# Optimization experiments

Hardware: AMD Instinct MI355X
Metric: run time of the kernel (lower is better)

Reference implementation:

```python
import math
import jax, jax.numpy as jnp
import numpy as np

B, T, C = 4, 2048, 1024
N_HEAD = 16
HEAD_DIM = C // N_HEAD

def setup_inputs() -> dict:
    key = jax.random.key(0)
    k0, k1, k2, k3, k4 = jax.random.split(key, 5)
    s = 1.0 / math.sqrt(C)
    return {
        "x": jax.random.normal(k0, (B, T, C), dtype=jnp.float32),
        "W_q": jax.random.normal(k1, (C, C), dtype=jnp.float32) * s,
        "W_k": jax.random.normal(k2, (C, C), dtype=jnp.float32) * s,
        "W_v": jax.random.normal(k3, (C, C), dtype=jnp.float32) * s,
        "W_o": jax.random.normal(k4, (C, C), dtype=jnp.float32) * s,
    }

def reference(x, W_q, W_k, W_v, W_o):
    b, t, c = x.shape
    h, hd = N_HEAD, HEAD_DIM
    # nn.Linear(y) = y @ W.T ; project and split heads -> [B, H, T, hd]
    q = (x @ W_q.T).reshape(b, t, h, hd).transpose(0, 2, 1, 3)
    k = (x @ W_k.T).reshape(b, t, h, hd).transpose(0, 2, 1, 3)
    v = (x @ W_v.T).reshape(b, t, h, hd).transpose(0, 2, 1, 3)
    # scores [B, H, T, T], causal mask, stable softmax
    attn = jnp.einsum('bhqd,bhkd->bhqk', q, k) / math.sqrt(hd)
    causal = jnp.tril(jnp.ones((t, t), dtype=bool))
    attn = jnp.where(causal[None, None], attn, -jnp.inf)
    attn = jax.nn.softmax(attn, axis=-1)
    out = jnp.einsum('bhqk,bhkd->bhqd', attn, v)
    out = out.transpose(0, 2, 1, 3).reshape(b, t, c)
    return out @ W_o.T
```

## Files before the change

kernel.cpp:

```cpp
#include <hip/hip_runtime.h>
#include <math.h>

#define Bsz 4
#define Tsz 2048
#define Csz 1024
#define NH  16
#define HD  64

typedef short bf16x8 __attribute__((ext_vector_type(8)));
typedef float f32x4  __attribute__((ext_vector_type(4)));
typedef unsigned short u16;
typedef unsigned int uint;

__device__ __forceinline__ u16 f2bf(float f) {
    union { float f; unsigned u; } v; v.f = f;
    unsigned r = v.u + 0x7fffu + ((v.u >> 16) & 1u);
    return (u16)(r >> 16);
}

__device__ __forceinline__ uint pkbf(float a, float b) {
    union { float f; uint u; } x, y; x.f = a; y.f = b;
    return ((x.u + 0x8000u) >> 16) | ((y.u + 0x8000u) & 0xFFFF0000u);
}

__device__ __forceinline__ void glds16(const u16* g, u16* l) {
    __builtin_amdgcn_global_load_lds(
        (const __attribute__((address_space(1))) void*)g,
        (__attribute__((address_space(3))) void*)l, 16, 0, 0);
}

__global__ void cast_kernel(const float* __restrict__ src, u16* __restrict__ dst, int n) {
    int i = (blockIdx.x * blockDim.x + threadIdx.x) * 8;
    if (i + 8 <= n) {
        float4 a = *(const float4*)(src + i);
        float4 b = *(const float4*)(src + i + 4);
        bf16x8 o;
        o[0] = (short)f2bf(a.x); o[1] = (short)f2bf(a.y);
        o[2] = (short)f2bf(a.z); o[3] = (short)f2bf(a.w);
        o[4] = (short)f2bf(b.x); o[5] = (short)f2bf(b.y);
        o[6] = (short)f2bf(b.z); o[7] = (short)f2bf(b.w);
        *(bf16x8*)(dst + i) = o;
    } else {
        for (; i < n; i++) dst[i] = f2bf(src[i]);
    }
}

__global__ void cast4_kernel(const float* __restrict__ s0, const float* __restrict__ s1,
                             const float* __restrict__ s2, const float* __restrict__ s3,
                             u16* __restrict__ dst) {
    const int NW = Csz * Csz;
    int i = (blockIdx.x * blockDim.x + threadIdx.x) * 8;
    int m = i >> 20;
    int local = i & (NW - 1);
    const float* src = (m == 0) ? s0 : (m == 1) ? s1 : (m == 2) ? s2 : s3;
    float4 a = *(const float4*)(src + local);
    float4 b = *(const float4*)(src + local + 4);
    bf16x8 o;
    o[0] = (short)f2bf(a.x); o[1] = (short)f2bf(a.y);
    o[2] = (short)f2bf(a.z); o[3] = (short)f2bf(a.w);
    o[4] = (short)f2bf(b.x); o[5] = (short)f2bf(b.y);
    o[6] = (short)f2bf(b.z); o[7] = (short)f2bf(b.w);
    *(bf16x8*)(dst + i) = o;
}


#define G8_SLOTSZ 32768
#define G8_MATSZ  16384
#define G8_KHSZ    8192

#define G8_STAGE(SLOT, MAT, KH, KT, PTR)                                             \
    { _Pragma("unroll")                                                              \
      for (int rho = 0; rho < 2; rho++) {                                            \
        const int row = rho * 128 + (tid >> 2);                                      \
        const int sc = (tid & 3) ^ ((row >> 1) & 3);                                 \
        glds16((PTR) + (size_t)row * 1024 + (KT) * 64 + (KH) * 32 + sc * 8,          \
               lds + (SLOT) * G8_SLOTSZ + (MAT) * G8_MATSZ + (KH) * G8_KHSZ +        \
                     rho * 4096 + wave * 512);                                       \
    } }

#define G8_PHASE(SLOT, KH, MH, STAGE)                                                \
    {                                                                                \
        __builtin_amdgcn_s_barrier();                                                \
        asm volatile("" ::: "memory");                                               \
        STAGE                                                                        \
        const u16* abase = lds + (SLOT) * G8_SLOTSZ + (KH) * G8_KHSZ;                \
        const u16* bbase = abase + G8_MATSZ;                                         \
        if ((MH) == 0) {                                                             \
            _Pragma("unroll")                                                        \
            for (int j = 0; j < 4; j++) {                                            \
                const int nr = wcb + j * 16 + lr;                                    \
                bfrag[j] = *(const bf16x8*)(bbase + nr * 32 +                        \
                                            ((lq ^ ((nr >> 1) & 3)) * 8));           \
            }                                                                        \
        }                                                                            \
        bf16x8 afr[4];                                                               \
        _Pragma("unroll")                                                            \
        for (int i = 0; i < 4; i++) {                                                \
            const int ar = wrb + ((MH) * 4 + i) * 16 + lr;                           \
            afr[i] = *(const bf16x8*)(abase + ar * 32 +                              \
                                      ((lq ^ ((ar >> 1) & 3)) * 8));                 \
        }                                                                            \
        asm volatile("" ::: "memory");                                               \
        __builtin_amdgcn_s_setprio(1);                                               \
        _Pragma("unroll")                                                            \
        for (int i = 0; i < 4; i++)                                                  \
            _Pragma("unroll")                                                        \
            for (int j = 0; j < 4; j++)                                              \
                acc[(MH) * 4 + i][j] = __builtin_amdgcn_mfma_f32_16x16x32_bf16(      \
                    afr[i], bfrag[j], acc[(MH) * 4 + i][j], 0, 0, 0);                \
        __builtin_amdgcn_s_setprio(0);                                               \
    }

#define G8_VM(N) asm volatile("s_waitcnt vmcnt(" #N ")" ::: "memory")

#define G8_BODY(AP_, BP_)                                                            \
    __shared__ u16 lds[65536];                                                       \
    const int tid = threadIdx.x;                                                     \
    const int wave = tid >> 6, lane = tid & 63;                                      \
    const int lr = lane & 15, lq = lane >> 4;                                        \
    const int wrb = (wave >> 2) * 128, wcb = (wave & 3) * 64;                        \
    f32x4 acc[8][4] = {};                                                            \
    bf16x8 bfrag[4];                                                                 \
    G8_STAGE(0, 0, 0, 0, AP_) G8_STAGE(0, 1, 0, 0, BP_)                              \
    G8_STAGE(0, 0, 1, 0, AP_) G8_STAGE(0, 1, 1, 0, BP_)                              \
    G8_STAGE(1, 0, 0, 1, AP_) G8_STAGE(1, 1, 0, 1, BP_)                              \
    for (int t = 0; t < 16; t++) {                                                   \
        const int s = t & 1;                                                         \
        if (t == 15) { G8_VM(4); } else { G8_VM(8); }                                \
        G8_PHASE(s, 0, 0, if (t < 15) G8_STAGE(s ^ 1, 0, 1, t + 1, AP_))             \
        G8_PHASE(s, 0, 1, if (t < 15) G8_STAGE(s ^ 1, 1, 1, t + 1, BP_))             \
        if (t == 15) { G8_VM(0); } else { G8_VM(8); }                                \
        G8_PHASE(s, 1, 0, if (t < 14) G8_STAGE(s, 0, 0, t + 2, AP_))                 \
        G8_PHASE(s, 1, 1, if (t < 14) G8_STAGE(s, 1, 0, t + 2, BP_))                 \
    }

__global__ __launch_bounds__(512, 2)
void gemm_qkv(const u16* __restrict__ A, const u16* __restrict__ Bm,
              u16* __restrict__ Qo, u16* __restrict__ Ko, u16* __restrict__ Vo,
              float qscale) {
    const int wg = blockIdx.x;
    const int chunk = wg & 7, pos = wg >> 3;
    const int m0 = ((chunk >> 1) * 8 + pos / 6) * 256;
    const int n0 = ((chunk & 1) * 6 + pos % 6) * 256;
    const u16* Ap = A  + (size_t)m0 * 1024;
    const u16* Bp = Bm + (size_t)n0 * 1024;

    G8_BODY(Ap, Bp)

    const int sel = n0 >> 10;
    if (sel == 2) {
        #pragma unroll
        for (int mi = 0; mi < 8; mi++) {
            #pragma unroll
            for (int ni = 0; ni < 4; ni++) {
                int m = m0 + wrb + mi * 16 + lq * 4;
                int b = m >> 11, tt = m & (Tsz - 1);
                int n = (n0 & 1023) + wcb + ni * 16 + lr;
                int h = n >> 6, d = n & (HD - 1);
                uint2 pk;
                pk.x = pkbf(acc[mi][ni][0], acc[mi][ni][1]);
                pk.y = pkbf(acc[mi][ni][2], acc[mi][ni][3]);
                *(uint2*)(&Vo[(((size_t)b * NH + h) * HD + d) * Tsz + tt]) = pk;
            }
        }
    } else {
        const float scale = (sel == 0) ? qscale : 1.0f;
        u16* dst = (sel == 0) ? Qo : Ko;
        #pragma unroll
        for (int mi = 0; mi < 8; mi++)
            #pragma unroll
            for (int ni = 0; ni < 4; ni++)
                #pragma unroll
                for (int r = 0; r < 4; r++) {
                    int m = m0 + wrb + mi * 16 + lq * 4 + r;
                    int n = (n0 & 1023) + wcb + ni * 16 + lr;
                    int b = m >> 11, tt = m & (Tsz - 1);
                    int h = n >> 6,  d = n & (HD - 1);
                    dst[(((size_t)b * NH + h) * Tsz + tt) * HD + d] = f2bf(acc[mi][ni][r] * scale);
                }
    }
}

__global__ __launch_bounds__(512, 2)
void gemm_out(const u16* __restrict__ A, const u16* __restrict__ Bm,
              float* __restrict__ out) {
    const int wg = blockIdx.x;
    const int chunk = wg & 7, pos = wg >> 3;
    const int m0 = (chunk * 4 + (pos >> 2)) * 256;
    const int n0 = (pos & 3) * 256;
    const u16* Ap = A  + (size_t)m0 * 1024;
    const u16* Bp = Bm + (size_t)n0 * 1024;

    G8_BODY(Ap, Bp)

    #pragma unroll
    for (int mi = 0; mi < 8; mi++)
        #pragma unroll
        for (int ni = 0; ni < 4; ni++)
            #pragma unroll
            for (int r = 0; r < 4; r++) {
                int m = m0 + wrb + mi * 16 + lq * 4 + r;
                int n = n0 + wcb + ni * 16 + lr;
                out[(size_t)m * Csz + n] = acc[mi][ni][r];
            }
}

#define LDT  72
#define LDTP 68

__global__ __launch_bounds__(256, 4)
void attn_kernel(const u16* __restrict__ Q, const u16* __restrict__ Kb,
                 const u16* __restrict__ Vt, u16* __restrict__ O) {
    __shared__ u16 sK[64 * LDT];
    __shared__ u16 sV[64 * LDT];
    __shared__ u16 sP[4][16 * LDTP];
    const int tid  = threadIdx.x;
    const int wave = tid >> 6, lane = tid & 63;
    const int lr = lane & 15, lq = lane >> 4;
    const int bh = blockIdx.x;
    const int qa = blockIdx.y;
    const int qc = 31 - qa;
    const int ta = qa * 64, tc = qc * 64;

    const u16* Qp = Q  + (size_t)bh * Tsz * HD;
    const u16* Kp = Kb + (size_t)bh * Tsz * HD;
    const u16* Vp = Vt + (size_t)bh * HD * Tsz;

    bf16x8 qfA0 = *(const bf16x8*)(Qp + (size_t)(ta + wave * 16 + lr) * HD + lq * 8);
    bf16x8 qfA1 = *(const bf16x8*)(Qp + (size_t)(ta + wave * 16 + lr) * HD + 32 + lq * 8);
    bf16x8 qfC0 = *(const bf16x8*)(Qp + (size_t)(tc + wave * 16 + lr) * HD + lq * 8);
    bf16x8 qfC1 = *(const bf16x8*)(Qp + (size_t)(tc + wave * 16 + lr) * HD + 32 + lq * 8);

    f32x4 accOA[4] = {}, accOC[4] = {};
    f32x4 accLA = {}, accLC = {};

    bf16x8 ones;
    #pragma unroll
    for (int i = 0; i < 8; i++) ones[i] = (short)0x3F80;

    const int strow = tid >> 3;
    const int stcol = (tid & 7) * 8;
    const u16* gK0 = Kp + (size_t)strow * HD + stcol;
    const u16* gK1 = gK0 + 32 * HD;
    const u16* gV0 = Vp + (size_t)strow * Tsz + stcol;
    const u16* gV1 = gV0 + 32 * Tsz;
    u16* lK0 = sK + strow * LDT + stcol;  u16* lK1 = lK0 + 32 * LDT;
    u16* lV0 = sV + strow * LDT + stcol;  u16* lV1 = lV0 + 32 * LDT;

    bf16x8 pK0 = *(const bf16x8*)(gK0);
    bf16x8 pK1 = *(const bf16x8*)(gK1);
    bf16x8 pV0 = *(const bf16x8*)(gV0);
    bf16x8 pV1 = *(const bf16x8*)(gV1);

#define PROCESS(T0, QF0, QF1, ACCO, ACCL, DIAG)                                       \
    {                                                                                 \
        f32x4 accS[4];                                                                \
        _Pragma("unroll")                                                             \
        for (int j = 0; j < 4; j++) {                                                 \
            bf16x8 b0 = *(const bf16x8*)(sK + (j * 16 + lr) * LDT + lq * 8);          \
            bf16x8 b1 = *(const bf16x8*)(sK + (j * 16 + lr) * LDT + 32 + lq * 8);     \
            f32x4 z = {};                                                             \
            z = __builtin_amdgcn_mfma_f32_16x16x32_bf16(QF0, b0, z, 0, 0, 0);         \
            z = __builtin_amdgcn_mfma_f32_16x16x32_bf16(QF1, b1, z, 0, 0, 0);         \
            accS[j] = z;                                                              \
        }                                                                             \
        _Pragma("unroll")                                                             \
        for (int r = 0; r < 4; r++) {                                                 \
            const int rowg = (T0) + wave * 16 + lq * 4 + r;                           \
            _Pragma("unroll")                                                         \
            for (int j = 0; j < 4; j++) {                                             \
                float v = accS[j][r];                                                 \
                if (DIAG && (kb * 64 + j * 16 + lr > rowg)) v = -200.0f;              \
                union { float f; uint u; } e;                                         \
                e.f = __builtin_amdgcn_exp2f(v);                                      \
                sP[wave][(lq * 4 + r) * LDTP + j * 16 + lr] = (u16)(e.u >> 16);       \
            }                                                                         \
        }                                                                             \
        _Pragma("unroll")                                                             \
        for (int ks = 0; ks < 2; ks++) {                                              \
            bf16x8 pf = *(const bf16x8*)(&sP[wave][0] + lr * LDTP + ks * 32 + lq * 8);\
            ACCL = __builtin_amdgcn_mfma_f32_16x16x32_bf16(pf, ones, ACCL, 0, 0, 0);  \
            _Pragma("unroll")                                                         \
            for (int j = 0; j < 4; j++) {                                             \
                bf16x8 vf = *(const bf16x8*)(sV + (j * 16 + lr) * LDT + ks * 32 + lq * 8); \
                ACCO[j] = __builtin_amdgcn_mfma_f32_16x16x32_bf16(pf, vf, ACCO[j], 0, 0, 0); \
            }                                                                         \
        }                                                                             \
    }

    for (int kb = 0; kb <= qc; kb++) {
        __syncthreads();
        *(bf16x8*)lK0 = pK0; *(bf16x8*)lK1 = pK1;
        *(bf16x8*)lV0 = pV0; *(bf16x8*)lV1 = pV1;
        __syncthreads();
        if (kb < qc) {
            pK0 = *(const bf16x8*)(gK0 + (size_t)(kb + 1) * 64 * HD);
            pK1 = *(const bf16x8*)(gK1 + (size_t)(kb + 1) * 64 * HD);
            pV0 = *(const bf16x8*)(gV0 + (kb + 1) * 64);
            pV1 = *(const bf16x8*)(gV1 + (kb + 1) * 64);
        }
        if (kb <= qa) PROCESS(ta, qfA0, qfA1, accOA, accLA, (kb == qa));
        PROCESS(tc, qfC0, qfC1, accOC, accLC, (kb == qc));
    }
#undef PROCESS

    const int b = bh >> 4, h = bh & 15;
    #pragma unroll
    for (int j = 0; j < 4; j++) {
        #pragma unroll
        for (int r = 0; r < 4; r++) {
            int t = wave * 16 + lq * 4 + r;
            int d = j * 16 + lr;
            O[((size_t)b * Tsz + ta + t) * Csz + h * HD + d] = f2bf(accOA[j][r] / accLA[r]);
            O[((size_t)b * Tsz + tc + t) * Csz + h * HD + d] = f2bf(accOC[j][r] / accLC[r]);
        }
    }
}

extern "C" void kernel_launch(void* const* d_in, const int* in_sizes, int n_in,
                              void* d_out, int out_size, void* d_ws, size_t ws_size,
                              hipStream_t stream) {
    const float* x  = (const float*)d_in[0];
    const float* Wq = (const float*)d_in[1];
    const float* Wk = (const float*)d_in[2];
    const float* Wv = (const float*)d_in[3];
    const float* Wo = (const float*)d_in[4];
    float* out = (float*)d_out;

    const size_t NX = (size_t)Bsz * Tsz * Csz;
    const size_t NW = (size_t)Csz * Csz;

    char* ws = (char*)d_ws;
    u16* xb   = (u16*)ws; ws += NX * 2;
    u16* wqkv = (u16*)ws; ws += 3 * NW * 2;
    u16* wob  = (u16*)ws; ws += NW * 2;
    u16* qbuf = (u16*)ws; ws += NX * 2;
    u16* kbuf = (u16*)ws; ws += NX * 2;
    u16* vtb  = (u16*)ws; ws += NX * 2;
    u16* abuf = (u16*)ws; ws += NX * 2;

    cast_kernel<<<dim3((unsigned)(NX / 2048)), 256, 0, stream>>>(x, xb, (int)NX);
    cast4_kernel<<<dim3((unsigned)(4 * NW / 2048)), 256, 0, stream>>>(Wq, Wk, Wv, Wo, wqkv);

    const float qscale = 0.125f * 1.44269504088896340736f;
    gemm_qkv<<<dim3(384), 512, 0, stream>>>(xb, wqkv, qbuf, kbuf, vtb, qscale);

    attn_kernel<<<dim3(Bsz * NH, 16), 256, 0, stream>>>(qbuf, kbuf, vtb, abuf);

    gemm_out<<<dim3(128), 512, 0, stream>>>(abuf, wob, out);
}
```

Baseline: 251.7 us.

## Shrink GEMM tiles to 128x256, raise priority on attention MFMAs, specialize diagonal branches

Both projection GEMMs change from 256x256 output tiles to 128x256, which halves the accumulators and LDS per workgroup and doubles the grid (768 and 256 blocks). The aim is to fill all CUs better, since the output GEMM previously launched only 128 blocks on a device with far more CUs. In exchange, each tile reuses less data per byte loaded. The attention kernel also wraps its MFMA sections in s_setprio and splits the per-block branch so the causal mask is compiled in only for diagonal blocks.

```diff
diff --git a/kernel.cpp b/kernel.cpp
--- a/kernel.cpp
+++ b/kernel.cpp
@@ -64,41 +64,41 @@
 }
 
 
-#define G8_SLOTSZ 32768
-#define G8_MATSZ  16384
-#define G8_KHSZ    8192
-
-#define G8_STAGE(SLOT, MAT, KH, KT, PTR)                                             \
-    { _Pragma("unroll")                                                              \
-      for (int rho = 0; rho < 2; rho++) {                                            \
-        const int row = rho * 128 + (tid >> 2);                                      \
-        const int sc = (tid & 3) ^ ((row >> 1) & 3);                                 \
-        glds16((PTR) + (size_t)row * 1024 + (KT) * 64 + (KH) * 32 + sc * 8,          \
-               lds + (SLOT) * G8_SLOTSZ + (MAT) * G8_MATSZ + (KH) * G8_KHSZ +        \
-                     rho * 4096 + wave * 512);                                       \
-    } }
-
-#define G8_PHASE(SLOT, KH, MH, STAGE)                                                \
+#define G2_SS 24576
+
+#define G2_STAGEA(SLOT, KH, KT, PTR) {                                               \
+    const int row_ = tid >> 2;                                                       \
+    const int sc_ = (tid & 3) ^ ((row_ >> 1) & 3);                                   \
+    glds16((PTR) + (size_t)row_ * 1024 + (KT) * 64 + (KH) * 32 + sc_ * 8,            \
+           lds + (SLOT) * G2_SS + (KH) * 4096 + wave * 512); }
+
+#define G2_STAGEB(SLOT, KH, KT, PTR) {                                               \
+    _Pragma("unroll")                                                                \
+    for (int rho = 0; rho < 2; rho++) {                                              \
+        const int row_ = rho * 128 + (tid >> 2);                                     \
+        const int sc_ = (tid & 3) ^ ((row_ >> 1) & 3);                               \
+        glds16((PTR) + (size_t)row_ * 1024 + (KT) * 64 + (KH) * 32 + sc_ * 8,        \
+               lds + (SLOT) * G2_SS + 8192 + (KH) * 8192 + rho * 4096 + wave * 512); } }
+
+#define G2_PHASE(SLOT, KH, STAGE)                                                    \
     {                                                                                \
         __builtin_amdgcn_s_barrier();                                                \
         asm volatile("" ::: "memory");                                               \
         STAGE                                                                        \
-        const u16* abase = lds + (SLOT) * G8_SLOTSZ + (KH) * G8_KHSZ;                \
-        const u16* bbase = abase + G8_MATSZ;                                         \
-        if ((MH) == 0) {                                                             \
-            _Pragma("unroll")                                                        \
-            for (int j = 0; j < 4; j++) {                                            \
-                const int nr = wcb + j * 16 + lr;                                    \
-                bfrag[j] = *(const bf16x8*)(bbase + nr * 32 +                        \
-                                            ((lq ^ ((nr >> 1) & 3)) * 8));           \
-            }                                                                        \
-        }                                                                            \
-        bf16x8 afr[4];                                                               \
+        const u16* abase = lds + (SLOT) * G2_SS + (KH) * 4096;                       \
+        const u16* bbase = lds + (SLOT) * G2_SS + 8192 + (KH) * 8192;                \
+        bf16x8 afr[4], bfr[4];                                                       \
         _Pragma("unroll")                                                            \
         for (int i = 0; i < 4; i++) {                                                \
-            const int ar = wrb + ((MH) * 4 + i) * 16 + lr;                           \
+            const int ar = wrb + i * 16 + lr;                                        \
             afr[i] = *(const bf16x8*)(abase + ar * 32 +                              \
                                       ((lq ^ ((ar >> 1) & 3)) * 8));                 \
+        }                                                                            \
+        _Pragma("unroll")                                                            \
+        for (int j = 0; j < 4; j++) {                                                \
+            const int nr = wcb + j * 16 + lr;                                        \
+            bfr[j] = *(const bf16x8*)(bbase + nr * 32 +                              \
+                                      ((lq ^ ((nr >> 1) & 3)) * 8));                 \
         }                                                                            \
         asm volatile("" ::: "memory");                                               \
         __builtin_amdgcn_s_setprio(1);                                               \
@@ -106,32 +106,31 @@
         for (int i = 0; i < 4; i++)                                                  \
             _Pragma("unroll")                                                        \
             for (int j = 0; j < 4; j++)                                              \
-                acc[(MH) * 4 + i][j] = __builtin_amdgcn_mfma_f32_16x16x32_bf16(      \
-                    afr[i], bfrag[j], acc[(MH) * 4 + i][j], 0, 0, 0);                \
+                acc[i][j] = __builtin_amdgcn_mfma_f32_16x16x32_bf16(                 \
+                    afr[i], bfr[j], acc[i][j], 0, 0, 0);                             \
         __builtin_amdgcn_s_setprio(0);                                               \
     }
 
-#define G8_VM(N) asm volatile("s_waitcnt vmcnt(" #N ")" ::: "memory")
-
-#define G8_BODY(AP_, BP_)                                                            \
-    __shared__ u16 lds[65536];                                                       \
+#define G2_VM(N) asm volatile("s_waitcnt vmcnt(" #N ")" ::: "memory")
+
+#define G2_BODY(AP_, BP_)                                                            \
+    __shared__ u16 lds[49152];                                                       \
     const int tid = threadIdx.x;                                                     \
     const int wave = tid >> 6, lane = tid & 63;                                      \
     const int lr = lane & 15, lq = lane >> 4;                                        \
-    const int wrb = (wave >> 2) * 128, wcb = (wave & 3) * 64;                        \
-    f32x4 acc[8][4] = {};                                                            \
-    bf16x8 bfrag[4];                                                                 \
-    G8_STAGE(0, 0, 0, 0, AP_) G8_STAGE(0, 1, 0, 0, BP_)                              \
-    G8_STAGE(0, 0, 1, 0, AP_) G8_STAGE(0, 1, 1, 0, BP_)                              \
-    G8_STAGE(1, 0, 0, 1, AP_) G8_STAGE(1, 1, 0, 1, BP_)                              \
+    const int wrb = (wave >> 2) * 64, wcb = (wave & 3) * 64;                         \
+    f32x4 acc[4][4] = {};                                                            \
+    G2_STAGEA(0, 0, 0, AP_) G2_STAGEB(0, 0, 0, BP_)                                  \
+    G2_STAGEA(0, 1, 0, AP_) G2_STAGEB(0, 1, 0, BP_)                                  \
+    G2_STAGEA(1, 0, 1, AP_) G2_STAGEB(1, 0, 1, BP_)                                  \
     for (int t = 0; t < 16; t++) {                                                   \
         const int s = t & 1;                                                         \
-        if (t == 15) { G8_VM(4); } else { G8_VM(8); }                                \
-        G8_PHASE(s, 0, 0, if (t < 15) G8_STAGE(s ^ 1, 0, 1, t + 1, AP_))             \
-        G8_PHASE(s, 0, 1, if (t < 15) G8_STAGE(s ^ 1, 1, 1, t + 1, BP_))             \
-        if (t == 15) { G8_VM(0); } else { G8_VM(8); }                                \
-        G8_PHASE(s, 1, 0, if (t < 14) G8_STAGE(s, 0, 0, t + 2, AP_))                 \
-        G8_PHASE(s, 1, 1, if (t < 14) G8_STAGE(s, 1, 0, t + 2, BP_))                 \
+        if (t == 15) { G2_VM(3); } else { G2_VM(6); }                                \
+        G2_PHASE(s, 0, if (t < 15) { G2_STAGEA(s ^ 1, 1, t + 1, AP_)                 \
+                                     G2_STAGEB(s ^ 1, 1, t + 1, BP_) })              \
+        if (t == 15) { G2_VM(0); } else { G2_VM(6); }                                \
+        G2_PHASE(s, 1, if (t < 14) { G2_STAGEA(s, 0, t + 2, AP_)                     \
+                                     G2_STAGEB(s, 0, t + 2, BP_) })                  \
     }
 
 __global__ __launch_bounds__(512, 2)
@@ -140,17 +139,17 @@
               float qscale) {
     const int wg = blockIdx.x;
     const int chunk = wg & 7, pos = wg >> 3;
-    const int m0 = ((chunk >> 1) * 8 + pos / 6) * 256;
+    const int m0 = ((chunk >> 1) * 16 + pos / 6) * 128;
     const int n0 = ((chunk & 1) * 6 + pos % 6) * 256;
     const u16* Ap = A  + (size_t)m0 * 1024;
     const u16* Bp = Bm + (size_t)n0 * 1024;
 
-    G8_BODY(Ap, Bp)
+    G2_BODY(Ap, Bp)
 
     const int sel = n0 >> 10;
     if (sel == 2) {
         #pragma unroll
-        for (int mi = 0; mi < 8; mi++) {
+        for (int mi = 0; mi < 4; mi++) {
             #pragma unroll
             for (int ni = 0; ni < 4; ni++) {
                 int m = m0 + wrb + mi * 16 + lq * 4;
@@ -167,7 +166,7 @@
         const float scale = (sel == 0) ? qscale : 1.0f;
         u16* dst = (sel == 0) ? Qo : Ko;
         #pragma unroll
-        for (int mi = 0; mi < 8; mi++)
+        for (int mi = 0; mi < 4; mi++)
             #pragma unroll
             for (int ni = 0; ni < 4; ni++)
                 #pragma unroll
@@ -186,15 +185,15 @@
               float* __restrict__ out) {
     const int wg = blockIdx.x;
     const int chunk = wg & 7, pos = wg >> 3;
-    const int m0 = (chunk * 4 + (pos >> 2)) * 256;
+    const int m0 = (chunk * 8 + (pos >> 2)) * 128;
     const int n0 = (pos & 3) * 256;
     const u16* Ap = A  + (size_t)m0 * 1024;
     const u16* Bp = Bm + (size_t)n0 * 1024;
 
-    G8_BODY(Ap, Bp)
+    G2_BODY(Ap, Bp)
 
     #pragma unroll
-    for (int mi = 0; mi < 8; mi++)
+    for (int mi = 0; mi < 4; mi++)
         #pragma unroll
         for (int ni = 0; ni < 4; ni++)
             #pragma unroll
@@ -255,6 +254,7 @@
 #define PROCESS(T0, QF0, QF1, ACCO, ACCL, DIAG)                                       \
     {                                                                                 \
         f32x4 accS[4];                                                                \
+        __builtin_amdgcn_s_setprio(1);                                                \
         _Pragma("unroll")                                                             \
         for (int j = 0; j < 4; j++) {                                                 \
             bf16x8 b0 = *(const bf16x8*)(sK + (j * 16 + lr) * LDT + lq * 8);          \
@@ -264,6 +264,7 @@
             z = __builtin_amdgcn_mfma_f32_16x16x32_bf16(QF1, b1, z, 0, 0, 0);         \
             accS[j] = z;                                                              \
         }                                                                             \
+        __builtin_amdgcn_s_setprio(0);                                                \
         _Pragma("unroll")                                                             \
         for (int r = 0; r < 4; r++) {                                                 \
             const int rowg = (T0) + wave * 16 + lq * 4 + r;                           \
@@ -276,6 +277,7 @@
                 sP[wave][(lq * 4 + r) * LDTP + j * 16 + lr] = (u16)(e.u >> 16);       \
             }                                                                         \
         }                                                                             \
+        __builtin_amdgcn_s_setprio(1);                                                \
         _Pragma("unroll")                                                             \
         for (int ks = 0; ks < 2; ks++) {                                              \
             bf16x8 pf = *(const bf16x8*)(&sP[wave][0] + lr * LDTP + ks * 32 + lq * 8);\
@@ -286,6 +288,7 @@
                 ACCO[j] = __builtin_amdgcn_mfma_f32_16x16x32_bf16(pf, vf, ACCO[j], 0, 0, 0); \
             }                                                                         \
         }                                                                             \
+        __builtin_amdgcn_s_setprio(0);                                                \
     }
 
     for (int kb = 0; kb <= qc; kb++) {
@@ -299,8 +302,17 @@
             pV0 = *(const bf16x8*)(gV0 + (kb + 1) * 64);
             pV1 = *(const bf16x8*)(gV1 + (kb + 1) * 64);
         }
-        if (kb <= qa) PROCESS(ta, qfA0, qfA1, accOA, accLA, (kb == qa));
-        PROCESS(tc, qfC0, qfC1, accOC, accLC, (kb == qc));
+        if (kb < qa) {
+            PROCESS(ta, qfA0, qfA1, accOA, accLA, 0)
+            PROCESS(tc, qfC0, qfC1, accOC, accLC, 0)
+        } else if (kb == qa) {
+            PROCESS(ta, qfA0, qfA1, accOA, accLA, 1)
+            PROCESS(tc, qfC0, qfC1, accOC, accLC, 0)
+        } else if (kb < qc) {
+            PROCESS(tc, qfC0, qfC1, accOC, accLC, 0)
+        } else {
+            PROCESS(tc, qfC0, qfC1, accOC, accLC, 1)
+        }
     }
 #undef PROCESS
 
@@ -343,9 +355,9 @@
     cast4_kernel<<<dim3((unsigned)(4 * NW / 2048)), 256, 0, stream>>>(Wq, Wk, Wv, Wo, wqkv);
 
     const float qscale = 0.125f * 1.44269504088896340736f;
-    gemm_qkv<<<dim3(384), 512, 0, stream>>>(xb, wqkv, qbuf, kbuf, vtb, qscale);
+    gemm_qkv<<<dim3(768), 512, 0, stream>>>(xb, wqkv, qbuf, kbuf, vtb, qscale);
 
     attn_kernel<<<dim3(Bsz * NH, 16), 256, 0, stream>>>(qbuf, kbuf, vtb, abuf);
 
-    gemm_out<<<dim3(128), 512, 0, stream>>>(abuf, wob, out);
-}
+    gemm_out<<<dim3(256), 512, 0, stream>>>(abuf, wob, out);
+}
```

New measurement: 258.1 us. 1.03x slower.
